# Optimization experiments

Hardware: AMD Instinct MI355X
Metric: run time of the kernel (lower is better)

## Reference

```python
import jax, jax.numpy as jnp
import numpy as np

B, S, C = 16, 4096, 512   # genes, splice sites per gene, site rep channels
J = 4096                  # unique junctions per gene
T, K = 64, 32             # transcripts per gene, junctions per transcript
H = 1024                  # layer_channels; in_channels = 2*C = 1024
STD = 0.02                # config.initializer_range


def setup_inputs() -> dict:
    key = jax.random.key(0)
    ks = jax.random.split(key, 8)
    return {
        "splice_site_reps": jax.random.normal(ks[0], (B, S, C), jnp.float32),
        # indices in [0, S+2): values S -> gene_start token, S+1 -> gene_end token
        "don_idx": jax.random.randint(ks[1], (B, J), 0, S + 2, jnp.int32),
        "acc_idx": jax.random.randint(ks[2], (B, J), 0, S + 2, jnp.int32),
        "transcript_junctions": jax.random.randint(ks[3], (B, T, K), 0, J, jnp.int32),
        "W1": jax.random.normal(ks[4], (2 * C, H), jnp.float32) * STD,
        "b1": jnp.zeros((H,), jnp.float32),
        "W2": jax.random.normal(ks[5], (H, H), jnp.float32) * STD,
        "b2": jnp.zeros((H,), jnp.float32),
        "W3": jax.random.normal(ks[6], (H, 1), jnp.float32) * STD,
        "b3": jnp.zeros((1,), jnp.float32),
        "gene_start_rep": jnp.zeros((C,), jnp.float32),
        "gene_end_rep": jnp.zeros((C,), jnp.float32),
        "ref_potential": jnp.zeros((1,), jnp.float32),
    }


def reference(splice_site_reps, don_idx, acc_idx, transcript_junctions,
              W1, b1, W2, b2, W3, b3,
              gene_start_rep, gene_end_rep, ref_potential):
    b = splice_site_reps.shape[0]
    # augment per-gene site table with gene_start / gene_end reps -> [B, S+2, C]
    aug = jnp.concatenate([
        splice_site_reps,
        jnp.broadcast_to(gene_start_rep, (b, 1, C)),
        jnp.broadcast_to(gene_end_rep, (b, 1, C)),
    ], axis=1)
    don_emb = jnp.take_along_axis(aug, don_idx[:, :, None], axis=1)   # [B,J,C]
    acc_emb = jnp.take_along_axis(aug, acc_idx[:, :, None], axis=1)   # [B,J,C]
    x = jnp.concatenate([don_emb, acc_emb], axis=-1)                  # [B,J,2C]
    # SpliceosomeNet: Linear-ReLU-Linear-ReLU-Linear(->1)
    h = jax.nn.relu(x @ W1 + b1)
    h = jax.nn.relu(h @ W2 + b2)
    pot = (h @ W3 + b3)[..., 0]                                       # [B,J]
    # transcript total potential = sum of its junction potentials
    tj = transcript_junctions.reshape(b, T * K)
    tpot = jnp.take_along_axis(pot, tj, axis=1).reshape(b, T, K).sum(-1)  # [B,T]
    all_pot = jnp.concatenate([tpot, jnp.broadcast_to(ref_potential, (b, 1))], axis=1)
    return jax.nn.softmax(all_pot, axis=-1)                           # [B,T+1]
```

## Files before the change

### kernel.cpp

```cpp
#include <hip/hip_runtime.h>
#include <hip/hip_bf16.h>
#include <stdint.h>
#include <stddef.h>

#define NB 16
#define NS 4096
#define NSA 4098
#define SFS 4104
#define NC 512
#define NJ 4096
#define NT 64
#define NKJ 32
#define KD 1024

#define NJC 2048
#define NMC (NB * NJC)

#define P0_COMPACT_BLKS NB
#define P0_W_BLKS 2048
#define P0_POT_BLKS 8
#define AUG_BLKS ((NB * NSA) / 4)

typedef __hip_bfloat16 bf16;
typedef __attribute__((ext_vector_type(8))) short bf16x8;
typedef __attribute__((ext_vector_type(4))) float f32x4;

#define BM 128
#define BN 128
#define BK 64

__device__ __forceinline__ void gload_lds16(const bf16* g, bf16* l) {
  __builtin_amdgcn_global_load_lds(
      (const __attribute__((address_space(1))) void*)g,
      (__attribute__((address_space(3))) void*)l, 16, 0, 0);
}

__device__ __forceinline__ void tile_from_bid(int bid, int& row_idx,
                                              int& col_idx) {
  row_idx = ((bid >> 6) << 3) | (bid & 7);
  col_idx = (bid >> 3) & 7;
}

__device__ __forceinline__ int map_tile(const int* __restrict__ cnt,
                                        int row_tile, int& b_out) {
  int at = 0;
#pragma unroll
  for (int b = 0; b < NB; b++) {
    const int g = (cnt[b] + (BM - 1)) >> 7;
    if (row_tile < at + g) { b_out = b; return row_tile - at; }
    at += g;
  }
  b_out = -1;
  return 0;
}

__global__ __launch_bounds__(1024) void prep0_kernel(
    const int* __restrict__ tj,
    const int* __restrict__ don,
    const int* __restrict__ acc,
    int* __restrict__ rows_list,
    int* __restrict__ pmap,
    int* __restrict__ cnt,
    unsigned char* __restrict__ sflag,
    const float* __restrict__ W1, bf16* __restrict__ W1t,
    const float* __restrict__ W2, bf16* __restrict__ W2t,
    float* __restrict__ pot) {
  const int bid = blockIdx.x;
  const int tid = threadIdx.x;
  if (bid < P0_COMPACT_BLKS) {
    const int b = bid;
    const int lane = tid & 63;
    const int wv = tid >> 6;
    __shared__ unsigned char flg[NJ];
    __shared__ int wtot[16];

    *(uint32_t*)&flg[tid * 4] = 0u;
    unsigned char* sf = sflag + (size_t)b * SFS;
    ((uint32_t*)sf)[tid] = 0u;
    if (tid < SFS / 4 - 1024) ((uint32_t*)sf)[1024 + tid] = 0u;
    __syncthreads();

#pragma unroll
    for (int k = 0; k < 2; k++) {
      const int j = tj[b * (NT * NKJ) + tid * 2 + k];
      flg[j] = 1;
    }
    if (tid == 0) flg[0] = 1;
    __syncthreads();

    const int j0 = tid * 4;
    const int f0 = flg[j0], f1 = flg[j0 + 1], f2 = flg[j0 + 2],
              f3 = flg[j0 + 3];
    const int ls = f0 + f1 + f2 + f3;

    int x = ls;
#pragma unroll
    for (int o = 1; o < 64; o <<= 1) {
      const int y = __shfl_up(x, o);
      if (lane >= o) x += y;
    }
    if (lane == 63) wtot[wv] = x;
    __syncthreads();

    int woff = 0, total = 0;
#pragma unroll
    for (int w = 0; w < 16; w++) {
      const int t = wtot[w];
      if (w < wv) woff += t;
      total += t;
    }
    int p = woff + x - ls;

    const int* donb = don + (size_t)b * NJ;
    const int* accb = acc + (size_t)b * NJ;
    int* rl = rows_list + (size_t)b * NJC;
    int* pm = pmap + (size_t)b * NJ;
    if (f0) { rl[p] = j0;     pm[j0]     = p; sf[donb[j0]]     = 1; sf[accb[j0]]     = 1; p++; }
    if (f1) { rl[p] = j0 + 1; pm[j0 + 1] = p; sf[donb[j0 + 1]] = 1; sf[accb[j0 + 1]] = 1; p++; }
    if (f2) { rl[p] = j0 + 2; pm[j0 + 2] = p; sf[donb[j0 + 2]] = 1; sf[accb[j0 + 2]] = 1; p++; }
    if (f3) { rl[p] = j0 + 3; pm[j0 + 3] = p; sf[donb[j0 + 3]] = 1; sf[accb[j0 + 3]] = 1; p++; }

    for (int i = total + tid; i < NJC; i += 1024) rl[i] = 0;
    if (tid == 0) cnt[b] = total;
  } else if (bid < P0_COMPACT_BLKS + P0_W_BLKS) {
    __shared__ bf16 tile[32][33];
    const int pos0 = bid - P0_COMPACT_BLKS;
    const float* W = (pos0 >= 1024) ? W2 : W1;
    bf16* Wt = (pos0 >= 1024) ? W2t : W1t;
    const int pos = pos0 & 1023;
    const int n0 = (pos & 31) * 32;
    const int k0 = (pos >> 5) * 32;
    const int c = tid & 31;
    const int r = tid >> 5;
    tile[r][c] = __float2bfloat16(W[(size_t)(k0 + r) * KD + (n0 + c)]);
    __syncthreads();
    Wt[(size_t)(n0 + r) * KD + (k0 + c)] = tile[c][r];
  } else {
    const int i = (bid - (P0_COMPACT_BLKS + P0_W_BLKS)) * 4096 + tid * 4;
    *(f32x4*)(pot + i) = (f32x4){0.f, 0.f, 0.f, 0.f};
  }
}

__global__ void aug_prep_kernel(const float* __restrict__ ssr,
                                const float* __restrict__ gstart,
                                const float* __restrict__ gend,
                                const unsigned char* __restrict__ sflag,
                                bf16* __restrict__ aug) {
  const int row = blockIdx.x * 4 + (threadIdx.x >> 6);
  const int i = threadIdx.x & 63;
  const int b = row / NSA;
  const int s = row - b * NSA;
  if (!sflag[(size_t)b * SFS + s]) return;
  const float* src;
  if (s < NS)       src = ssr + ((size_t)b * NS + s) * NC;
  else if (s == NS) src = gstart;
  else              src = gend;
  f32x4 f0 = *(const f32x4*)(src + 4 * i);
  f32x4 f1 = *(const f32x4*)(src + 256 + 4 * i);
  bf16* dst = aug + (size_t)row * NC;
  union { uint64_t u; bf16 e[4]; } a, b4;
  a.e[0] = __float2bfloat16(f0.x); a.e[1] = __float2bfloat16(f0.y);
  a.e[2] = __float2bfloat16(f0.z); a.e[3] = __float2bfloat16(f0.w);
  b4.e[0] = __float2bfloat16(f1.x); b4.e[1] = __float2bfloat16(f1.y);
  b4.e[2] = __float2bfloat16(f1.z); b4.e[3] = __float2bfloat16(f1.w);
  *(uint64_t*)(dst + 4 * i) = a.u;
  *(uint64_t*)(dst + 256 + 4 * i) = b4.u;
}

__global__ __launch_bounds__(256, 2) void gemm1_gather_kernel(
    const bf16* __restrict__ aug, const int* __restrict__ don,
    const int* __restrict__ acc, const int* __restrict__ rows_list,
    const int* __restrict__ cnt, const bf16* __restrict__ Bt,
    const float* __restrict__ bias, bf16* __restrict__ Cout) {
  __shared__ __align__(16) bf16 As[BM * BK];
  __shared__ __align__(16) bf16 Bs[BN * BK];
  const int tid = threadIdx.x;
  const int wave = tid >> 6;
  const int lane = tid & 63;
  int row_idx, col_idx;
  tile_from_bid(blockIdx.x, row_idx, col_idx);
  int gb;
  const int lt = map_tile(cnt, row_idx, gb);
  if (gb < 0) return;
  const int grow0 = gb * NJC + lt * BM;
  const int col0 = col_idx * BN;
  const int wm = wave & 1;
  const int wn = wave >> 1;
  const int q = lane >> 4;
  const int rr = lane & 15;

  int mm[4], gg[4];
#pragma unroll
  for (int i = 0; i < 4; i++) {
    int L = wave * 256 + i * 64 + lane;
    int m = L >> 3;
    int g = (L & 7) ^ (m & 7);
    mm[i] = m; gg[i] = g;
  }

  const bf16* dp[4];
  const bf16* ap[4];
#pragma unroll
  for (int i = 0; i < 4; i++) {
    const int jid = rows_list[grow0 + mm[i]];
    dp[i] = aug + ((size_t)gb * NSA + don[gb * NJ + jid]) * NC;
    ap[i] = aug + ((size_t)gb * NSA + acc[gb * NJ + jid]) * NC;
  }

  f32x4 acc4[4][4] = {};

  for (int kt = 0; kt < KD / BK; ++kt) {
    const int ko = (kt & 7) * BK;
#pragma unroll
    for (int i = 0; i < 4; i++) {
      const bf16* abase = (kt < 8) ? dp[i] : ap[i];
      gload_lds16(abase + ko + gg[i] * 8,
                  As + (size_t)(wave * 256 + i * 64) * 8);
      gload_lds16(Bt + ((size_t)(col0 + mm[i]) * KD + kt * BK + gg[i] * 8),
                  Bs + (size_t)(wave * 256 + i * 64) * 8);
    }
    __syncthreads();
#pragma unroll
    for (int kk = 0; kk < 2; ++kk) {
      bf16x8 afr[4], bfr[4];
      const int g = kk * 4 + q;
#pragma unroll
      for (int mt = 0; mt < 4; mt++) {
        int m = wm * 64 + mt * 16 + rr;
        afr[mt] = *(const bf16x8*)(As + (m * 8 + (g ^ (m & 7))) * 8);
      }
#pragma unroll
      for (int nt = 0; nt < 4; nt++) {
        int n = wn * 64 + nt * 16 + rr;
        bfr[nt] = *(const bf16x8*)(Bs + (n * 8 + (g ^ (n & 7))) * 8);
      }
#pragma unroll
      for (int mt = 0; mt < 4; mt++)
#pragma unroll
        for (int nt = 0; nt < 4; nt++)
          acc4[mt][nt] = __builtin_amdgcn_mfma_f32_16x16x32_bf16(
              afr[mt], bfr[nt], acc4[mt][nt], 0, 0, 0);
    }
    __syncthreads();
  }

#pragma unroll
  for (int nt = 0; nt < 4; nt++) {
    const int col = col0 + wn * 64 + nt * 16 + rr;
    const float bv = bias[col];
#pragma unroll
    for (int mt = 0; mt < 4; mt++) {
      const int rbase = grow0 + wm * 64 + mt * 16 + q * 4;
#pragma unroll
      for (int rg = 0; rg < 4; rg++) {
        float v = fmaxf(acc4[mt][nt][rg] + bv, 0.f);
        Cout[(size_t)(rbase + rg) * KD + col] = __float2bfloat16(v);
      }
    }
  }
}

__global__ __launch_bounds__(256, 2) void gemm2_kernel(
    const bf16* __restrict__ A, const int* __restrict__ cnt,
    const bf16* __restrict__ Bt, const float* __restrict__ bias,
    const float* __restrict__ w3, float* __restrict__ pot) {
  __shared__ __align__(16) bf16 As[BM * BK];
  __shared__ __align__(16) bf16 Bs[BN * BK];
  const int tid = threadIdx.x;
  const int wave = tid >> 6;
  const int lane = tid & 63;
  int row_idx, col_idx;
  tile_from_bid(blockIdx.x, row_idx, col_idx);
  int gb;
  const int lt = map_tile(cnt, row_idx, gb);
  if (gb < 0) return;
  const int grow0 = gb * NJC + lt * BM;
  const int col0 = col_idx * BN;
  const int wm = wave & 1;
  const int wn = wave >> 1;
  const int q = lane >> 4;
  const int rr = lane & 15;

  int mm[4], gg[4];
#pragma unroll
  for (int i = 0; i < 4; i++) {
    int L = wave * 256 + i * 64 + lane;
    int m = L >> 3;
    int g = (L & 7) ^ (m & 7);
    mm[i] = m; gg[i] = g;
  }

  f32x4 acc4[4][4] = {};

  for (int kt = 0; kt < KD / BK; ++kt) {
#pragma unroll
    for (int i = 0; i < 4; i++) {
      gload_lds16(A + ((size_t)(grow0 + mm[i]) * KD + kt * BK + gg[i] * 8),
                  As + (size_t)(wave * 256 + i * 64) * 8);
      gload_lds16(Bt + ((size_t)(col0 + mm[i]) * KD + kt * BK + gg[i] * 8),
                  Bs + (size_t)(wave * 256 + i * 64) * 8);
    }
    __syncthreads();
#pragma unroll
    for (int kk = 0; kk < 2; ++kk) {
      bf16x8 afr[4], bfr[4];
      const int g = kk * 4 + q;
#pragma unroll
      for (int mt = 0; mt < 4; mt++) {
        int m = wm * 64 + mt * 16 + rr;
        afr[mt] = *(const bf16x8*)(As + (m * 8 + (g ^ (m & 7))) * 8);
      }
#pragma unroll
      for (int nt = 0; nt < 4; nt++) {
        int n = wn * 64 + nt * 16 + rr;
        bfr[nt] = *(const bf16x8*)(Bs + (n * 8 + (g ^ (n & 7))) * 8);
      }
#pragma unroll
      for (int mt = 0; mt < 4; mt++)
#pragma unroll
        for (int nt = 0; nt < 4; nt++)
          acc4[mt][nt] = __builtin_amdgcn_mfma_f32_16x16x32_bf16(
              afr[mt], bfr[nt], acc4[mt][nt], 0, 0, 0);
    }
    __syncthreads();
  }

  float bv[4], wv[4];
#pragma unroll
  for (int nt = 0; nt < 4; nt++) {
    const int col = col0 + wn * 64 + nt * 16 + rr;
    bv[nt] = bias[col];
    wv[nt] = w3[col];
  }
#pragma unroll
  for (int mt = 0; mt < 4; mt++) {
#pragma unroll
    for (int rg = 0; rg < 4; rg++) {
      float s = 0.f;
#pragma unroll
      for (int nt = 0; nt < 4; nt++)
        s += fmaxf(acc4[mt][nt][rg] + bv[nt], 0.f) * wv[nt];
      s += __shfl_xor(s, 1);
      s += __shfl_xor(s, 2);
      s += __shfl_xor(s, 4);
      s += __shfl_xor(s, 8);
      if (rr == 0) {
        int row = grow0 + wm * 64 + mt * 16 + q * 4 + rg;
        atomicAdd(&pot[row], s);
      }
    }
  }
}

__global__ void transcript_softmax_kernel(const float* __restrict__ pot,
                                          const int* __restrict__ tj,
                                          const int* __restrict__ pmap,
                                          const float* __restrict__ b3,
                                          const float* __restrict__ refp,
                                          float* __restrict__ out) {
  const int b = blockIdx.x;
  const int t = threadIdx.x;
  const int* tjb = tj + ((size_t)b * NT + t) * NKJ;
  const int* pm = pmap + (size_t)b * NJ;
  const float* pb = pot + (size_t)b * NJC;
  float s = 0.f;
#pragma unroll
  for (int k = 0; k < NKJ; k++) s += pb[pm[tjb[k]]];
  s += (float)NKJ * b3[0];
  const float ref = refp[0];
  float m = fmaxf(s, ref);
#pragma unroll
  for (int o = 1; o < 64; o <<= 1) m = fmaxf(m, __shfl_xor(m, o));
  const float e = expf(s - m);
  float denom = e;
#pragma unroll
  for (int o = 1; o < 64; o <<= 1) denom += __shfl_xor(denom, o);
  const float eref = expf(ref - m);
  denom += eref;
  out[b * (NT + 1) + t] = e / denom;
  if (t == 0) out[b * (NT + 1) + NT] = eref / denom;
}

extern "C" void kernel_launch(void* const* d_in, const int* in_sizes, int n_in,
                              void* d_out, int out_size, void* d_ws,
                              size_t ws_size, hipStream_t stream) {
  const float* ssr    = (const float*)d_in[0];
  const int*   don    = (const int*)d_in[1];
  const int*   acc    = (const int*)d_in[2];
  const int*   tj     = (const int*)d_in[3];
  const float* W1     = (const float*)d_in[4];
  const float* b1     = (const float*)d_in[5];
  const float* W2     = (const float*)d_in[6];
  const float* b2     = (const float*)d_in[7];
  const float* W3     = (const float*)d_in[8];
  const float* b3     = (const float*)d_in[9];
  const float* gstart = (const float*)d_in[10];
  const float* gend   = (const float*)d_in[11];
  const float* refp   = (const float*)d_in[12];
  float* out = (float*)d_out;

  char* ws = (char*)d_ws;
  bf16* W1t = (bf16*)ws;                 ws += (size_t)KD * KD * 2;
  bf16* W2t = (bf16*)ws;                 ws += (size_t)KD * KD * 2;
  bf16* aug = (bf16*)ws;                 ws += (size_t)NB * NSA * NC * 2;
  bf16* H1  = (bf16*)ws;                 ws += (size_t)NMC * KD * 2;
  float* pot = (float*)ws;               ws += (size_t)NMC * 4;
  int* rows_list = (int*)ws;             ws += (size_t)NB * NJC * 4;
  int* pmap = (int*)ws;                  ws += (size_t)NB * NJ * 4;
  int* cnt = (int*)ws;                   ws += 64;
  unsigned char* sflag = (unsigned char*)ws;  ws += (size_t)NB * SFS;

  prep0_kernel<<<P0_COMPACT_BLKS + P0_W_BLKS + P0_POT_BLKS, 1024, 0, stream>>>(
      tj, don, acc, rows_list, pmap, cnt, sflag, W1, W1t, W2, W2t, pot);

  aug_prep_kernel<<<AUG_BLKS, 256, 0, stream>>>(ssr, gstart, gend, sflag, aug);

  gemm1_gather_kernel<<<(NMC / BM) * (KD / BN), 256, 0, stream>>>(
      aug, don, acc, rows_list, cnt, W1t, b1, H1);

  gemm2_kernel<<<(NMC / BM) * (KD / BN), 256, 0, stream>>>(H1, cnt, W2t, b2,
                                                           W3, pot);

  transcript_softmax_kernel<<<NB, 64, 0, stream>>>(pot, tj, pmap, b3, refp,
                                                   out);
}
```

Measured before the change: 336.2 us.

## Fuse fp32-to-bf16 site gather into GEMM1, drop aug prep kernel

Removes the separate aug_prep kernel and the site-usage flag marking. GEMM1 now reads fp32 splice-site rows directly, including the gene start/end vectors, converts them to bf16 in registers and stores them to LDS. This saves a kernel launch plus the write and re-read of the bf16 staging table. In exchange, each row is re-read in fp32 once per column tile (8 times), and the A path becomes a synchronous register load instead of an async global-to-LDS copy.

```diff
diff --git a/kernel.cpp b/kernel.cpp
--- a/kernel.cpp
+++ b/kernel.cpp
@@ -6,7 +6,6 @@
 #define NB 16
 #define NS 4096
 #define NSA 4098
-#define SFS 4104
 #define NC 512
 #define NJ 4096
 #define NT 64
@@ -19,7 +18,6 @@
 #define P0_COMPACT_BLKS NB
 #define P0_W_BLKS 2048
 #define P0_POT_BLKS 8
-#define AUG_BLKS ((NB * NSA) / 4)
 
 typedef __hip_bfloat16 bf16;
 typedef __attribute__((ext_vector_type(8))) short bf16x8;
@@ -56,12 +54,9 @@
 
 __global__ __launch_bounds__(1024) void prep0_kernel(
     const int* __restrict__ tj,
-    const int* __restrict__ don,
-    const int* __restrict__ acc,
     int* __restrict__ rows_list,
     int* __restrict__ pmap,
     int* __restrict__ cnt,
-    unsigned char* __restrict__ sflag,
     const float* __restrict__ W1, bf16* __restrict__ W1t,
     const float* __restrict__ W2, bf16* __restrict__ W2t,
     float* __restrict__ pot) {
@@ -75,9 +70,6 @@
     __shared__ int wtot[16];
 
     *(uint32_t*)&flg[tid * 4] = 0u;
-    unsigned char* sf = sflag + (size_t)b * SFS;
-    ((uint32_t*)sf)[tid] = 0u;
-    if (tid < SFS / 4 - 1024) ((uint32_t*)sf)[1024 + tid] = 0u;
     __syncthreads();
 
 #pragma unroll
@@ -111,14 +103,12 @@
     }
     int p = woff + x - ls;
 
-    const int* donb = don + (size_t)b * NJ;
-    const int* accb = acc + (size_t)b * NJ;
     int* rl = rows_list + (size_t)b * NJC;
     int* pm = pmap + (size_t)b * NJ;
-    if (f0) { rl[p] = j0;     pm[j0]     = p; sf[donb[j0]]     = 1; sf[accb[j0]]     = 1; p++; }
-    if (f1) { rl[p] = j0 + 1; pm[j0 + 1] = p; sf[donb[j0 + 1]] = 1; sf[accb[j0 + 1]] = 1; p++; }
-    if (f2) { rl[p] = j0 + 2; pm[j0 + 2] = p; sf[donb[j0 + 2]] = 1; sf[accb[j0 + 2]] = 1; p++; }
-    if (f3) { rl[p] = j0 + 3; pm[j0 + 3] = p; sf[donb[j0 + 3]] = 1; sf[accb[j0 + 3]] = 1; p++; }
+    if (f0) { rl[p] = j0;     pm[j0]     = p; p++; }
+    if (f1) { rl[p] = j0 + 1; pm[j0 + 1] = p; p++; }
+    if (f2) { rl[p] = j0 + 2; pm[j0 + 2] = p; p++; }
+    if (f3) { rl[p] = j0 + 3; pm[j0 + 3] = p; p++; }
 
     for (int i = total + tid; i < NJC; i += 1024) rl[i] = 0;
     if (tid == 0) cnt[b] = total;
@@ -141,34 +131,9 @@
   }
 }
 
-__global__ void aug_prep_kernel(const float* __restrict__ ssr,
-                                const float* __restrict__ gstart,
-                                const float* __restrict__ gend,
-                                const unsigned char* __restrict__ sflag,
-                                bf16* __restrict__ aug) {
-  const int row = blockIdx.x * 4 + (threadIdx.x >> 6);
-  const int i = threadIdx.x & 63;
-  const int b = row / NSA;
-  const int s = row - b * NSA;
-  if (!sflag[(size_t)b * SFS + s]) return;
-  const float* src;
-  if (s < NS)       src = ssr + ((size_t)b * NS + s) * NC;
-  else if (s == NS) src = gstart;
-  else              src = gend;
-  f32x4 f0 = *(const f32x4*)(src + 4 * i);
-  f32x4 f1 = *(const f32x4*)(src + 256 + 4 * i);
-  bf16* dst = aug + (size_t)row * NC;
-  union { uint64_t u; bf16 e[4]; } a, b4;
-  a.e[0] = __float2bfloat16(f0.x); a.e[1] = __float2bfloat16(f0.y);
-  a.e[2] = __float2bfloat16(f0.z); a.e[3] = __float2bfloat16(f0.w);
-  b4.e[0] = __float2bfloat16(f1.x); b4.e[1] = __float2bfloat16(f1.y);
-  b4.e[2] = __float2bfloat16(f1.z); b4.e[3] = __float2bfloat16(f1.w);
-  *(uint64_t*)(dst + 4 * i) = a.u;
-  *(uint64_t*)(dst + 256 + 4 * i) = b4.u;
-}
-
 __global__ __launch_bounds__(256, 2) void gemm1_gather_kernel(
-    const bf16* __restrict__ aug, const int* __restrict__ don,
+    const float* __restrict__ ssr, const float* __restrict__ gstart,
+    const float* __restrict__ gend, const int* __restrict__ don,
     const int* __restrict__ acc, const int* __restrict__ rows_list,
     const int* __restrict__ cnt, const bf16* __restrict__ Bt,
     const float* __restrict__ bias, bf16* __restrict__ Cout) {
@@ -198,13 +163,17 @@
     mm[i] = m; gg[i] = g;
   }
 
-  const bf16* dp[4];
-  const bf16* ap[4];
+  const float* dp[4];
+  const float* ap[4];
 #pragma unroll
   for (int i = 0; i < 4; i++) {
     const int jid = rows_list[grow0 + mm[i]];
-    dp[i] = aug + ((size_t)gb * NSA + don[gb * NJ + jid]) * NC;
-    ap[i] = aug + ((size_t)gb * NSA + acc[gb * NJ + jid]) * NC;
+    const int sd = don[gb * NJ + jid];
+    const int sa = acc[gb * NJ + jid];
+    dp[i] = (sd < NS) ? ssr + ((size_t)gb * NS + sd) * NC
+                      : ((sd == NS) ? gstart : gend);
+    ap[i] = (sa < NS) ? ssr + ((size_t)gb * NS + sa) * NC
+                      : ((sa == NS) ? gstart : gend);
   }
 
   f32x4 acc4[4][4] = {};
@@ -213,11 +182,24 @@
     const int ko = (kt & 7) * BK;
 #pragma unroll
     for (int i = 0; i < 4; i++) {
-      const bf16* abase = (kt < 8) ? dp[i] : ap[i];
-      gload_lds16(abase + ko + gg[i] * 8,
-                  As + (size_t)(wave * 256 + i * 64) * 8);
       gload_lds16(Bt + ((size_t)(col0 + mm[i]) * KD + kt * BK + gg[i] * 8),
                   Bs + (size_t)(wave * 256 + i * 64) * 8);
+    }
+    f32x4 v0[4], v1[4];
+#pragma unroll
+    for (int i = 0; i < 4; i++) {
+      const float* base = ((kt < 8) ? dp[i] : ap[i]) + ko + gg[i] * 8;
+      v0[i] = *(const f32x4*)(base);
+      v1[i] = *(const f32x4*)(base + 4);
+    }
+#pragma unroll
+    for (int i = 0; i < 4; i++) {
+      union { bf16x8 v; bf16 e[8]; } u;
+      u.e[0] = __float2bfloat16(v0[i].x); u.e[1] = __float2bfloat16(v0[i].y);
+      u.e[2] = __float2bfloat16(v0[i].z); u.e[3] = __float2bfloat16(v0[i].w);
+      u.e[4] = __float2bfloat16(v1[i].x); u.e[5] = __float2bfloat16(v1[i].y);
+      u.e[6] = __float2bfloat16(v1[i].z); u.e[7] = __float2bfloat16(v1[i].w);
+      *(bf16x8*)(As + (size_t)(wave * 256 + i * 64 + lane) * 8) = u.v;
     }
     __syncthreads();
 #pragma unroll
@@ -402,21 +384,17 @@
   char* ws = (char*)d_ws;
   bf16* W1t = (bf16*)ws;                 ws += (size_t)KD * KD * 2;
   bf16* W2t = (bf16*)ws;                 ws += (size_t)KD * KD * 2;
-  bf16* aug = (bf16*)ws;                 ws += (size_t)NB * NSA * NC * 2;
   bf16* H1  = (bf16*)ws;                 ws += (size_t)NMC * KD * 2;
   float* pot = (float*)ws;               ws += (size_t)NMC * 4;
   int* rows_list = (int*)ws;             ws += (size_t)NB * NJC * 4;
   int* pmap = (int*)ws;                  ws += (size_t)NB * NJ * 4;
   int* cnt = (int*)ws;                   ws += 64;
-  unsigned char* sflag = (unsigned char*)ws;  ws += (size_t)NB * SFS;
 
   prep0_kernel<<<P0_COMPACT_BLKS + P0_W_BLKS + P0_POT_BLKS, 1024, 0, stream>>>(
-      tj, don, acc, rows_list, pmap, cnt, sflag, W1, W1t, W2, W2t, pot);
-
-  aug_prep_kernel<<<AUG_BLKS, 256, 0, stream>>>(ssr, gstart, gend, sflag, aug);
+      tj, rows_list, pmap, cnt, W1, W1t, W2, W2t, pot);
 
   gemm1_gather_kernel<<<(NMC / BM) * (KD / BN), 256, 0, stream>>>(
-      aug, don, acc, rows_list, cnt, W1t, b1, H1);
+      ssr, gstart, gend, don, acc, rows_list, cnt, W1t, b1, H1);
 
   gemm2_kernel<<<(NMC / BM) * (KD / BN), 256, 0, stream>>>(H1, cnt, W2t, b2,
                                                            W3, pot);
```

After: 361.4 us. +7.5%, slower.
